# Optimization experiments

Measured on AMD Instinct MI355X. Metric: run time of the kernel, lower is better.

The kernel has to match this reference:

```python
import jax, jax.numpy as jnp
import numpy as np
import math

B, S, H = 2, 2048, 2048
NH, LD = 16, 512
HD = H // NH


def setup_inputs() -> dict:
    key = jax.random.key(0)
    ks = jax.random.split(key, 9)
    sc = 0.02
    return {
        "x": jax.random.normal(ks[0], (B, S, H), dtype=jnp.float32),
        "wq": jax.random.normal(ks[1], (H, H), dtype=jnp.float32) * sc,
        "bq": jnp.zeros((H,), dtype=jnp.float32),
        "wk_lat": jax.random.normal(ks[2], (H, LD), dtype=jnp.float32) * sc,
        "wv_lat": jax.random.normal(ks[3], (H, LD), dtype=jnp.float32) * sc,
        "wk": jax.random.normal(ks[4], (LD, H), dtype=jnp.float32) * sc,
        "wv": jax.random.normal(ks[5], (LD, H), dtype=jnp.float32) * sc,
        "wo": jax.random.normal(ks[6], (H, H), dtype=jnp.float32) * sc,
        "bo": jnp.zeros((H,), dtype=jnp.float32),
    }


def reference(x, wq, bq, wk_lat, wv_lat, wk, wv, wo, bo):
    b, s, _ = x.shape
    # projections
    q = (x @ wq + bq).reshape(b, s, NH, HD).transpose(0, 2, 1, 3)  # [B,NH,S,HD]
    k_lat = x @ wk_lat  # [B,S,LD]
    v_lat = x @ wv_lat
    k = (k_lat @ wk).reshape(b, s, NH, HD).transpose(0, 2, 1, 3)
    v = (v_lat @ wv).reshape(b, s, NH, HD).transpose(0, 2, 1, 3)
    # causal attention
    scores = jnp.einsum('bhqd,bhkd->bhqk', q, k) / math.sqrt(HD)
    mask = jnp.tril(jnp.ones((s, s), dtype=bool))  # True = keep
    scores = jnp.where(mask, scores, -jnp.inf)
    weights = jax.nn.softmax(scores, axis=-1)
    out = jnp.einsum('bhqk,bhkd->bhqd', weights, v)
    out = out.transpose(0, 2, 1, 3).reshape(b, s, H)
    return out @ wo + bo
```

## Files before the change

kernel.cpp:

```cpp
#include <hip/hip_runtime.h>
#include <hip/hip_bf16.h>

#define PB   2
#define PS   2048
#define PH   2048
#define PNH  16
#define PLD  512
#define PHD  128
#define PM   (PB * PS)
#define PNCAT 3072
#define ATT_SCALE 0.08838834764831845f
#define ATT_MOFF 4.0f

typedef __attribute__((ext_vector_type(8))) short bf16x8;
typedef __attribute__((ext_vector_type(4))) float f32x4;

__device__ __forceinline__ unsigned short f2bf(float f) {
    unsigned int u = __float_as_uint(f);
    u += 0x7FFFu + ((u >> 16) & 1u);
    return (unsigned short)(u >> 16);
}

__device__ __forceinline__ void gl_lds16(const unsigned short* g, unsigned short* l) {
    __builtin_amdgcn_global_load_lds(
        (const __attribute__((address_space(1))) unsigned int*)g,
        (__attribute__((address_space(3))) unsigned int*)l, 16, 0, 0);
}

#define VMCNT(n)   asm volatile("s_waitcnt vmcnt(" #n ")" ::: "memory")
#define LGKM0()    asm volatile("s_waitcnt lgkmcnt(0)" ::: "memory")
#define MEMFENCE() asm volatile("" ::: "memory")

__global__ __launch_bounds__(256) void cast_f32_bf16_kernel(
    const float* __restrict__ in, unsigned short* __restrict__ out, int n)
{
    int i = (blockIdx.x * 256 + threadIdx.x) * 4;
    if (i >= n) return;
    float4 f = *(const float4*)(in + i);
    unsigned int a = (unsigned int)f2bf(f.x) | ((unsigned int)f2bf(f.y) << 16);
    unsigned int b = (unsigned int)f2bf(f.z) | ((unsigned int)f2bf(f.w) << 16);
    *(uint2*)(out + i) = make_uint2(a, b);
}

__global__ __launch_bounds__(256) void transpose_cast_kernel(
    const float* __restrict__ in, unsigned short* __restrict__ out, int R, int C)
{
    __shared__ float tile[32][33];
    int tx = threadIdx.x, ty = threadIdx.y;
    int r0 = blockIdx.y * 32, c0 = blockIdx.x * 32;
#pragma unroll
    for (int i = 0; i < 32; i += 8)
        tile[ty + i][tx] = in[(size_t)(r0 + ty + i) * C + (c0 + tx)];
    __syncthreads();
#pragma unroll
    for (int i = 0; i < 32; i += 8)
        out[(size_t)(c0 + ty + i) * R + (r0 + tx)] = f2bf(tile[tx][ty + i]);
}

template<int BM, int EPI, bool HAS_BIAS>
__global__ __launch_bounds__(512, 2) void gemm8p_kernel(
    const unsigned short* __restrict__ A, int lda,
    const unsigned short* __restrict__ BT,
    const float* __restrict__ bias, int nbias,
    void* __restrict__ Cout, int ldc, int K)
{
    constexpr int AH  = BM / 128;
    constexpr int MR  = BM / 32;
    constexpr int MH  = MR / 2;
    constexpr int ASZ = BM * 64;
    __shared__ __align__(16) unsigned short lds[2 * ASZ + 32768];

    const int tid  = threadIdx.x;
    const int wave = tid >> 6, lane = tid & 63;
    const int wm = wave >> 2, wn = wave & 3;
    const int quad = lane >> 4, l15 = lane & 15;
    const int sw = l15 & 7;

    const int gx  = gridDim.x;
    const int nwg = gx * gridDim.y;
    int wg = blockIdx.y * gx + blockIdx.x;
    if (!(nwg & 7)) wg = (wg & 7) * (nwg >> 3) + (wg >> 3);
    const int bm = (wg / gx) * BM, bn = (wg % gx) * 256;

    const int nt = K >> 6;

    const int srow = tid >> 3;
    const int scol = ((tid & 7) ^ (srow & 7)) << 3;
    const unsigned short* Ag = A  + (size_t)(bm + srow) * lda + scol;
    const unsigned short* Bg = BT + (size_t)(bn + srow) * K   + scol;
    unsigned short* const ldsA = &lds[wave * 512];
    unsigned short* const ldsB = &lds[2 * ASZ + wave * 512];

    auto stA = [&](int kt, int h, int b) {
        const unsigned short* g = Ag + (size_t)(h * 128) * lda + kt * 64;
        unsigned short* l = ldsA + b * ASZ + h * 8192;
        gl_lds16(g, l);
        gl_lds16(g + (size_t)64 * lda, l + 4096);
    };
    auto stB = [&](int kt, int h, int b) {
        const unsigned short* g = Bg + (size_t)(h * 128) * K + kt * 64;
        unsigned short* l = ldsB + b * 16384 + h * 8192;
        gl_lds16(g, l);
        gl_lds16(g + (size_t)64 * K, l + 4096);
    };

    auto ldA = [&](int b, int m, int ks) -> bf16x8 {
        int ra = wm * (BM / 2) + m * 16 + l15;
        return *(const bf16x8*)&lds[b * ASZ + (ra >> 7) * 8192 + (ra & 127) * 64
                                    + (((ks * 4 + quad) ^ sw) << 3)];
    };
    auto ldB = [&](int b, int j, int ks) -> bf16x8 {
        int rb = wn * 64 + j * 16 + l15;
        return *(const bf16x8*)&lds[2 * ASZ + b * 16384 + (rb >> 7) * 8192 + (rb & 127) * 64
                                    + (((ks * 4 + quad) ^ sw) << 3)];
    };

    f32x4 acc[MR][4] = {};
    bf16x8 af[MH][2], bl[2][2], bh[2][2];

    stA(0, 0, 0);
    if constexpr (AH == 2) stA(0, 1, 0);
    stB(0, 0, 0);
    stB(0, 1, 0);
    if (nt > 1) { stA(1, 0, 1); VMCNT(2); } else { VMCNT(0); }
    __builtin_amdgcn_s_barrier();
    MEMFENCE();

    for (int t = 0; t < nt; ++t) {
        const int b = t & 1, nb = b ^ 1;
        const bool s1 = (t + 1 < nt), s2 = (t + 2 < nt);

#pragma unroll
        for (int m = 0; m < MH; ++m)
#pragma unroll
            for (int ks = 0; ks < 2; ++ks) af[m][ks] = ldA(b, m, ks);
#pragma unroll
        for (int j = 0; j < 2; ++j)
#pragma unroll
            for (int ks = 0; ks < 2; ++ks) bl[j][ks] = ldB(b, j, ks);
        if (s1) { if constexpr (AH == 2) stA(t + 1, 1, nb); else stB(t + 1, 0, nb); }
        __builtin_amdgcn_s_barrier();
        LGKM0();
        __builtin_amdgcn_sched_barrier(0);
        __builtin_amdgcn_s_setprio(1);
#pragma unroll
        for (int m = 0; m < MH; ++m)
#pragma unroll
            for (int j = 0; j < 2; ++j)
#pragma unroll
                for (int ks = 0; ks < 2; ++ks)
                    acc[m][j] = __builtin_amdgcn_mfma_f32_16x16x32_bf16(af[m][ks], bl[j][ks], acc[m][j], 0, 0, 0);
        __builtin_amdgcn_s_setprio(0);
        __builtin_amdgcn_s_barrier();

#pragma unroll
        for (int j = 0; j < 2; ++j)
#pragma unroll
            for (int ks = 0; ks < 2; ++ks) bh[j][ks] = ldB(b, 2 + j, ks);
        if (s1) stB(t + 1, 1, nb);
        __builtin_amdgcn_s_barrier();
        LGKM0();
        __builtin_amdgcn_sched_barrier(0);
        __builtin_amdgcn_s_setprio(1);
#pragma unroll
        for (int m = 0; m < MH; ++m)
#pragma unroll
            for (int j = 0; j < 2; ++j)
#pragma unroll
                for (int ks = 0; ks < 2; ++ks)
                    acc[m][2 + j] = __builtin_amdgcn_mfma_f32_16x16x32_bf16(af[m][ks], bh[j][ks], acc[m][2 + j], 0, 0, 0);
        __builtin_amdgcn_s_setprio(0);
        __builtin_amdgcn_s_barrier();

#pragma unroll
        for (int m = 0; m < MH; ++m)
#pragma unroll
            for (int ks = 0; ks < 2; ++ks) af[m][ks] = ldA(b, MH + m, ks);
        if (s1) { if constexpr (AH == 2) stB(t + 1, 0, nb); }
        __builtin_amdgcn_s_barrier();
        LGKM0();
        __builtin_amdgcn_sched_barrier(0);
        __builtin_amdgcn_s_setprio(1);
#pragma unroll
        for (int m = 0; m < MH; ++m)
#pragma unroll
            for (int j = 0; j < 2; ++j)
#pragma unroll
                for (int ks = 0; ks < 2; ++ks)
                    acc[MH + m][2 + j] = __builtin_amdgcn_mfma_f32_16x16x32_bf16(af[m][ks], bh[j][ks], acc[MH + m][2 + j], 0, 0, 0);
        __builtin_amdgcn_s_setprio(0);
        __builtin_amdgcn_s_barrier();

#pragma unroll
        for (int j = 0; j < 2; ++j)
#pragma unroll
            for (int ks = 0; ks < 2; ++ks) bl[j][ks] = ldB(b, j, ks);
        if (s2) stA(t + 2, 0, b);
        __builtin_amdgcn_s_barrier();
        LGKM0();
        __builtin_amdgcn_sched_barrier(0);
        __builtin_amdgcn_s_setprio(1);
#pragma unroll
        for (int m = 0; m < MH; ++m)
#pragma unroll
            for (int j = 0; j < 2; ++j)
#pragma unroll
                for (int ks = 0; ks < 2; ++ks)
                    acc[MH + m][j] = __builtin_amdgcn_mfma_f32_16x16x32_bf16(af[m][ks], bl[j][ks], acc[MH + m][j], 0, 0, 0);
        __builtin_amdgcn_s_setprio(0);
        if (s2) { VMCNT(2); } else { VMCNT(0); }
        __builtin_amdgcn_s_barrier();
        MEMFENCE();
    }

#pragma unroll
    for (int m = 0; m < MR; ++m)
#pragma unroll
        for (int j = 0; j < 4; ++j)
#pragma unroll
            for (int r = 0; r < 4; ++r) {
                int row = bm + wm * (BM / 2) + m * 16 + quad * 4 + r;
                int col = bn + wn * 64 + j * 16 + l15;
                float val = acc[m][j][r];
                if (HAS_BIAS && col < nbias) val += bias[col];
                if (EPI == 2) {
                    int bb = row >> 11, s = row & 2047, hh = col >> 7, d = col & 127;
                    size_t idx = ((size_t)((bb << 4) + hh) << 18) + ((size_t)(s >> 6) << 13)
                               + ((d >> 3) << 9) + ((s & 63) << 3) + (d & 7);
                    ((unsigned short*)Cout)[idx] = f2bf(val);
                } else if (EPI == 3) {
                    int bb = row >> 11, s = row & 2047, hh = col >> 7, d = col & 127;
                    size_t idx = ((size_t)((bb << 4) + hh) << 18) + ((size_t)(s >> 6) << 13)
                               + (((s >> 3) & 7) << 10) + (d << 3) + (s & 7);
                    ((unsigned short*)Cout)[idx] = f2bf(val);
                } else if (EPI == 1) {
                    ((float*)Cout)[(size_t)row * ldc + col] = val;
                } else {
                    ((unsigned short*)Cout)[(size_t)row * ldc + col] = f2bf(val);
                }
            }
}

__global__ __launch_bounds__(256) void flash_attn_mfma_kernel(
    const unsigned short* __restrict__ q,
    const unsigned short* __restrict__ kswz,
    const unsigned short* __restrict__ vswz,
    unsigned short* __restrict__ o)
{
    __shared__ __align__(16) unsigned short Kl[2][8192];
    __shared__ __align__(16) unsigned short Vl[8192];
    __shared__ __align__(16) unsigned short Ps[4][16][72];

    const int tid  = threadIdx.x;
    const int wave = tid >> 6;
    const int lane = tid & 63;
    const int quad = lane >> 4, l15 = lane & 15;

    const int bid = blockIdx.x;
    const int qt = 31 - (bid >> 5);
    const int bh = bid & 31;
    const int b  = bh >> 4, h = bh & 15;
    const int q0 = qt * 64;

    const unsigned short* qbase = q + (size_t)(b * PS + q0) * PNCAT + h * PHD;
    const unsigned short* kbase = kswz + ((size_t)bh << 18);
    const unsigned short* vbase = vswz + ((size_t)bh << 18);

    auto stageK = [&](int it, int buf) {
        const unsigned short* kt = kbase + ((size_t)it << 13);
#pragma unroll
        for (int j = 0; j < 4; ++j)
            gl_lds16(kt + (wave * 4 + j) * 512 + lane * 8, &Kl[buf][(wave * 4 + j) * 512]);
    };
    auto stageV = [&](int it) {
        const unsigned short* vt = vbase + ((size_t)it << 13);
#pragma unroll
        for (int j = 0; j < 4; ++j)
            gl_lds16(vt + (wave * 4 + j) * 512 + lane * 8, &Vl[(wave * 4 + j) * 512]);
    };

    bf16x8 aq[4];
#pragma unroll
    for (int kk = 0; kk < 4; ++kk)
        aq[kk] = *(const bf16x8*)(qbase + (size_t)(wave * 16 + l15) * PNCAT + kk * 32 + quad * 8);

    bf16x8 vones;
#pragma unroll
    for (int j = 0; j < 8; ++j) vones[j] = (short)0x3F80;

    f32x4 oacc[8] = {};
    f32x4 lacc = {};

    stageK(0, 0);

    for (int it = 0; it <= qt; ++it) {
        const int cur = it & 1;
        __syncthreads();
        stageV(it);
        if (it < qt) stageK(it + 1, cur ^ 1);

        f32x4 sacc[4] = {};
#pragma unroll
        for (int kk = 0; kk < 4; ++kk)
#pragma unroll
            for (int n = 0; n < 4; ++n) {
                bf16x8 bk = *(const bf16x8*)&Kl[cur][((kk * 4 + quad) * 64 + n * 16 + l15) * 8];
                sacc[n] = __builtin_amdgcn_mfma_f32_16x16x32_bf16(aq[kk], bk, sacc[n], 0, 0, 0);
            }

        const bool diag = (it == qt);
#pragma unroll
        for (int n = 0; n < 4; ++n)
#pragma unroll
            for (int r = 0; r < 4; ++r) {
                float p = __expf(fmaf(sacc[n][r], ATT_SCALE, -ATT_MOFF));
                if (diag && (n * 16 + l15 > wave * 16 + quad * 4 + r)) p = 0.0f;
                Ps[wave][quad * 4 + r][n * 16 + l15] = f2bf(p);
            }

        __syncthreads();

#pragma unroll
        for (int kk = 0; kk < 2; ++kk) {
            bf16x8 ap = *(const bf16x8*)&Ps[wave][l15][kk * 32 + quad * 8];
            lacc = __builtin_amdgcn_mfma_f32_16x16x32_bf16(ap, vones, lacc, 0, 0, 0);
#pragma unroll
            for (int n = 0; n < 8; ++n) {
                bf16x8 bv = *(const bf16x8*)&Vl[((kk * 4 + quad) * 128 + n * 16 + l15) * 8];
                oacc[n] = __builtin_amdgcn_mfma_f32_16x16x32_bf16(ap, bv, oacc[n], 0, 0, 0);
            }
        }
    }

    float inv[4];
#pragma unroll
    for (int r = 0; r < 4; ++r) inv[r] = 1.0f / lacc[r];
#pragma unroll
    for (int n = 0; n < 8; ++n)
#pragma unroll
        for (int r = 0; r < 4; ++r) {
            int row = q0 + wave * 16 + quad * 4 + r;
            int col = h * PHD + n * 16 + l15;
            o[(size_t)(b * PS + row) * PH + col] = f2bf(oacc[n][r] * inv[r]);
        }
}

extern "C" void kernel_launch(void* const* d_in, const int* in_sizes, int n_in,
                              void* d_out, int out_size, void* d_ws, size_t ws_size,
                              hipStream_t stream)
{
    const float* x      = (const float*)d_in[0];
    const float* wq     = (const float*)d_in[1];
    const float* bq     = (const float*)d_in[2];
    const float* wk_lat = (const float*)d_in[3];
    const float* wv_lat = (const float*)d_in[4];
    const float* wk     = (const float*)d_in[5];
    const float* wv     = (const float*)d_in[6];
    const float* wo     = (const float*)d_in[7];
    const float* bo     = (const float*)d_in[8];
    float* out = (float*)d_out;

    char* ws = (char*)d_ws;
    size_t off = 0;
    auto alloc = [&](size_t bytes) -> void* {
        void* p = ws + off;
        off += (bytes + 255) & ~(size_t)255;
        return p;
    };
    unsigned short* xb    = (unsigned short*)alloc((size_t)PM * PH * 2);
    unsigned short* wcatT = (unsigned short*)alloc((size_t)PNCAT * PH * 2);
    unsigned short* wkT   = (unsigned short*)alloc((size_t)PH * PLD * 2);
    unsigned short* wvT   = (unsigned short*)alloc((size_t)PH * PLD * 2);
    unsigned short* woT   = (unsigned short*)alloc((size_t)PH * PH * 2);
    unsigned short* cat   = (unsigned short*)alloc((size_t)PM * PNCAT * 2);
    unsigned short* kswz  = (unsigned short*)alloc((size_t)PM * PH * 2);
    unsigned short* attn  = (unsigned short*)alloc((size_t)PM * PH * 2);
    unsigned short* vswz  = xb;

    unsigned short* wqT    = wcatT;
    unsigned short* wkLatT = wcatT + (size_t)PH * PH;
    unsigned short* wvLatT = wcatT + (size_t)(PH + PLD) * PH;

    dim3 tb(32, 8);

    cast_f32_bf16_kernel<<<(PM * PH) / 4 / 256, 256, 0, stream>>>(x, xb, PM * PH);
    transpose_cast_kernel<<<dim3(PH / 32,  PH / 32),  tb, 0, stream>>>(wq,     wqT,    PH,  PH);
    transpose_cast_kernel<<<dim3(PLD / 32, PH / 32),  tb, 0, stream>>>(wk_lat, wkLatT, PH,  PLD);
    transpose_cast_kernel<<<dim3(PLD / 32, PH / 32),  tb, 0, stream>>>(wv_lat, wvLatT, PH,  PLD);
    transpose_cast_kernel<<<dim3(PH / 32,  PLD / 32), tb, 0, stream>>>(wk,     wkT,    PLD, PH);
    transpose_cast_kernel<<<dim3(PH / 32,  PLD / 32), tb, 0, stream>>>(wv,     wvT,    PLD, PH);
    transpose_cast_kernel<<<dim3(PH / 32,  PH / 32),  tb, 0, stream>>>(wo,     woT,    PH,  PH);

    gemm8p_kernel<256, 0, true><<<dim3(PNCAT / 256, PM / 256), 512, 0, stream>>>(
        xb, PH, wcatT, bq, PH, cat, PNCAT, PH);

    gemm8p_kernel<128, 2, false><<<dim3(PH / 256, PM / 128), 512, 0, stream>>>(
        cat + PH, PNCAT, wkT, nullptr, 0, kswz, 0, PLD);
    gemm8p_kernel<128, 3, false><<<dim3(PH / 256, PM / 128), 512, 0, stream>>>(
        cat + PH + PLD, PNCAT, wvT, nullptr, 0, vswz, 0, PLD);

    flash_attn_mfma_kernel<<<PB * PNH * (PS / 64), 256, 0, stream>>>(cat, kswz, vswz, attn);

    gemm8p_kernel<128, 1, true><<<dim3(PH / 256, PM / 128), 512, 0, stream>>>(
        attn, PH, woT, bo, PH, out, PH, PH);
}
```

Baseline: 352.9 us.

## Interleave wave tile mapping and reorder GEMM global-to-LDS prefetch stages

The bf16 MFMA GEMM now gives each wave interleaved 16-row and 16-column slices instead of contiguous 64/128-row blocks. The global-to-LDS staging is split into 64-row chunks, so each compute phase only depends on the sub-tiles already loaded. Prefetch for tile t+2 starts earlier, A-lo in the third phase and A-hi/B-hi in the fourth, with wait counts raised to match. The goal is to overlap more load latency with MFMA work and spread VMEM issue more evenly. In exchange it carries more outstanding loads and relies on hand-tuned vmcnt values that must exactly match the issue order.

```diff
diff --git a/kernel.cpp b/kernel.cpp
--- a/kernel.cpp
+++ b/kernel.cpp
@@ -64,7 +64,6 @@
     const float* __restrict__ bias, int nbias,
     void* __restrict__ Cout, int ldc, int K)
 {
-    constexpr int AH  = BM / 128;
     constexpr int MR  = BM / 32;
     constexpr int MH  = MR / 2;
     constexpr int ASZ = BM * 64;
@@ -91,38 +90,38 @@
     unsigned short* const ldsA = &lds[wave * 512];
     unsigned short* const ldsB = &lds[2 * ASZ + wave * 512];
 
-    auto stA = [&](int kt, int h, int b) {
-        const unsigned short* g = Ag + (size_t)(h * 128) * lda + kt * 64;
-        unsigned short* l = ldsA + b * ASZ + h * 8192;
-        gl_lds16(g, l);
-        gl_lds16(g + (size_t)64 * lda, l + 4096);
-    };
-    auto stB = [&](int kt, int h, int b) {
-        const unsigned short* g = Bg + (size_t)(h * 128) * K + kt * 64;
-        unsigned short* l = ldsB + b * 16384 + h * 8192;
-        gl_lds16(g, l);
-        gl_lds16(g + (size_t)64 * K, l + 4096);
-    };
+    auto stA64 = [&](int kt, int sub, int b) {
+        gl_lds16(Ag + (size_t)(sub * 64) * lda + kt * 64, ldsA + b * ASZ + sub * 4096);
+    };
+    auto stB64 = [&](int kt, int sub, int b) {
+        gl_lds16(Bg + (size_t)(sub * 64) * K + kt * 64, ldsB + b * 16384 + sub * 4096);
+    };
+    auto stAlo = [&](int kt, int b) { stA64(kt, 0, b); if constexpr (BM == 256) stA64(kt, 1, b); };
+    auto stAhi = [&](int kt, int b) { if constexpr (BM == 256) { stA64(kt, 2, b); stA64(kt, 3, b); }
+                                      else stA64(kt, 1, b); };
+    auto stBlo = [&](int kt, int b) { stB64(kt, 0, b); stB64(kt, 1, b); };
+    auto stBhi = [&](int kt, int b) { stB64(kt, 2, b); stB64(kt, 3, b); };
 
     auto ldA = [&](int b, int m, int ks) -> bf16x8 {
-        int ra = wm * (BM / 2) + m * 16 + l15;
-        return *(const bf16x8*)&lds[b * ASZ + (ra >> 7) * 8192 + (ra & 127) * 64
-                                    + (((ks * 4 + quad) ^ sw) << 3)];
+        int ra = m * 32 + wm * 16 + l15;
+        return *(const bf16x8*)&lds[b * ASZ + ra * 64 + (((ks * 4 + quad) ^ sw) << 3)];
     };
     auto ldB = [&](int b, int j, int ks) -> bf16x8 {
-        int rb = wn * 64 + j * 16 + l15;
-        return *(const bf16x8*)&lds[2 * ASZ + b * 16384 + (rb >> 7) * 8192 + (rb & 127) * 64
-                                    + (((ks * 4 + quad) ^ sw) << 3)];
+        int rb = j * 64 + wn * 16 + l15;
+        return *(const bf16x8*)&lds[2 * ASZ + b * 16384 + rb * 64 + (((ks * 4 + quad) ^ sw) << 3)];
     };
 
     f32x4 acc[MR][4] = {};
     bf16x8 af[MH][2], bl[2][2], bh[2][2];
 
-    stA(0, 0, 0);
-    if constexpr (AH == 2) stA(0, 1, 0);
-    stB(0, 0, 0);
-    stB(0, 1, 0);
-    if (nt > 1) { stA(1, 0, 1); VMCNT(2); } else { VMCNT(0); }
+    stAlo(0, 0); stAhi(0, 0); stBlo(0, 0); stBhi(0, 0);
+    if (nt > 1) {
+        stAlo(1, 1);
+        stAhi(1, 1); stBhi(1, 1);
+        if constexpr (BM == 256) { VMCNT(6); } else { VMCNT(4); }
+    } else {
+        VMCNT(0);
+    }
     __builtin_amdgcn_s_barrier();
     MEMFENCE();
 
@@ -138,7 +137,7 @@
         for (int j = 0; j < 2; ++j)
 #pragma unroll
             for (int ks = 0; ks < 2; ++ks) bl[j][ks] = ldB(b, j, ks);
-        if (s1) { if constexpr (AH == 2) stA(t + 1, 1, nb); else stB(t + 1, 0, nb); }
+        if (s1) stBlo(t + 1, nb);
         __builtin_amdgcn_s_barrier();
         LGKM0();
         __builtin_amdgcn_sched_barrier(0);
@@ -157,7 +156,6 @@
         for (int j = 0; j < 2; ++j)
 #pragma unroll
             for (int ks = 0; ks < 2; ++ks) bh[j][ks] = ldB(b, 2 + j, ks);
-        if (s1) stB(t + 1, 1, nb);
         __builtin_amdgcn_s_barrier();
         LGKM0();
         __builtin_amdgcn_sched_barrier(0);
@@ -176,7 +174,7 @@
         for (int m = 0; m < MH; ++m)
 #pragma unroll
             for (int ks = 0; ks < 2; ++ks) af[m][ks] = ldA(b, MH + m, ks);
-        if (s1) { if constexpr (AH == 2) stB(t + 1, 0, nb); }
+        if (s2) stAlo(t + 2, b);
         __builtin_amdgcn_s_barrier();
         LGKM0();
         __builtin_amdgcn_sched_barrier(0);
@@ -195,7 +193,7 @@
         for (int j = 0; j < 2; ++j)
 #pragma unroll
             for (int ks = 0; ks < 2; ++ks) bl[j][ks] = ldB(b, j, ks);
-        if (s2) stA(t + 2, 0, b);
+        if (s2) { stAhi(t + 2, b); stBhi(t + 2, b); }
         __builtin_amdgcn_s_barrier();
         LGKM0();
         __builtin_amdgcn_sched_barrier(0);
@@ -208,7 +206,8 @@
                 for (int ks = 0; ks < 2; ++ks)
                     acc[MH + m][j] = __builtin_amdgcn_mfma_f32_16x16x32_bf16(af[m][ks], bl[j][ks], acc[MH + m][j], 0, 0, 0);
         __builtin_amdgcn_s_setprio(0);
-        if (s2) { VMCNT(2); } else { VMCNT(0); }
+        if (s2) { if constexpr (BM == 256) { VMCNT(6); } else { VMCNT(4); } }
+        else    { VMCNT(0); }
         __builtin_amdgcn_s_barrier();
         MEMFENCE();
     }
@@ -219,8 +218,8 @@
         for (int j = 0; j < 4; ++j)
 #pragma unroll
             for (int r = 0; r < 4; ++r) {
-                int row = bm + wm * (BM / 2) + m * 16 + quad * 4 + r;
-                int col = bn + wn * 64 + j * 16 + l15;
+                int row = bm + m * 32 + wm * 16 + quad * 4 + r;
+                int col = bn + j * 64 + wn * 16 + l15;
                 float val = acc[m][j][r];
                 if (HAS_BIAS && col < nbias) val += bias[col];
                 if (EPI == 2) {
```

New measurement: 352.6 us. No clear change (-0.1%).
